# Performance work log

Hardware: AMD Instinct MI355X
Metric: run time of the kernel (lower is better)

The kernel has to match this reference:

```python
import jax, jax.numpy as jnp
import numpy as np

F_CH = 12   # self.f
R = 2       # self.r
LN_EPS = 1e-5


def setup_inputs() -> dict:
    key = jax.random.key(0)
    ks = jax.random.split(key, 12)
    B, C, h, w = 1024, 200, 15, 15
    f, fr = F_CH, F_CH // R
    X = jax.random.normal(ks[0], (B, C, h, w), dtype=jnp.float32)
    # 1x1 conv weights stored as [out, in]; biases [out]
    s_in = 1.0 / np.sqrt(C)
    w11 = jax.random.normal(ks[1], (f, C), dtype=jnp.float32) * s_in
    b11 = jax.random.normal(ks[2], (f,), dtype=jnp.float32) * 0.01
    w21 = jax.random.normal(ks[3], (f, C), dtype=jnp.float32) * s_in
    b21 = jax.random.normal(ks[4], (f,), dtype=jnp.float32) * 0.01
    w31 = jax.random.normal(ks[5], (f, C), dtype=jnp.float32) * s_in
    b31 = jax.random.normal(ks[6], (f,), dtype=jnp.float32) * 0.01
    w41 = jax.random.normal(ks[7], (fr, f), dtype=jnp.float32) * (1.0 / np.sqrt(f))
    b41 = jax.random.normal(ks[8], (fr,), dtype=jnp.float32) * 0.01
    w42 = jax.random.normal(ks[9], (C, fr), dtype=jnp.float32) * (1.0 / np.sqrt(fr))
    b42 = jax.random.normal(ks[10], (C,), dtype=jnp.float32) * 0.01
    ln_g = jnp.ones((C,), dtype=jnp.float32)
    ln_b = jnp.zeros((C,), dtype=jnp.float32)
    return {"X": X, "w11": w11, "b11": b11, "w21": w21, "b21": b21,
            "w31": w31, "b31": b31, "w41": w41, "b41": b41,
            "w42": w42, "b42": b42, "ln_g": ln_g, "ln_b": ln_b}


def reference(X, w11, b11, w21, b21, w31, b31, w41, b41, w42, b42, ln_g, ln_b):
    B, C, h, w = X.shape
    f = F_CH
    HW = h * w
    Xf = X.reshape(B, C, HW)                       # flatten spatial for 1x1 convs
    k = jnp.einsum('bcn,fc->bfn', Xf, w11) + b11[:, None]   # [B,f,HW]
    q = jnp.einsum('bcn,fc->bfn', Xf, w21) + b21[:, None]
    kq = k * q                                               # [B,f,HW]
    v = jnp.einsum('bcn,fc->bfn', Xf, w31) + b31[:, None]    # [B,f,HW]
    # original: permute to [B,h,w,f] then raw reshape to [B,f,1,HW] (scrambles data)
    vp = jnp.transpose(v.reshape(B, f, h, w), (0, 2, 3, 1)).reshape(B, f, HW)
    vm = jnp.mean(vp, axis=-1)                               # adaptive avg pool -> [B,f]
    vs = jax.nn.softmax(vm, axis=1)                          # nn.Softmax default dim=1 on 4D
    # einsum 'bkij,blik->bijl' with i=1: out[b,j,l] = (sum_k kq[b,k,j]) * vs[b,l]
    kqs = jnp.sum(kq, axis=1)                                # [B,HW]
    x41 = kqs[:, :, None] * vs[:, None, :]                   # [B,HW,f]
    x = x41 @ w41.T + b41                                    # conv41: [B,HW,f//r]
    x = x @ w42.T + b42                                      # conv42: [B,HW,C]
    mu = jnp.mean(x, axis=-1, keepdims=True)
    var = jnp.var(x, axis=-1, keepdims=True)
    xn = (x - mu) / jnp.sqrt(var + LN_EPS) * ln_g + ln_b     # LayerNorm(C)
    x42 = jax.nn.sigmoid(jax.nn.relu(xn))                    # [B,HW,C]
    gate = jnp.transpose(x42, (0, 2, 1)).reshape(B, C, h, w)
    return gate * X
```

## Files before the change

kernel.cpp:

```cpp
#include <hip/hip_runtime.h>
#include <math.h>

#define F_CH 12
#define C_DIM 200
#define HW 225
#define PERB (C_DIM*HW)
#define PERB4 (PERB/4)
#define LN_EPS 1e-5f

#define WS_WT   0
#define WS_DP   7200
#define WS_VARD 7400

__global__ __launch_bounds__(256) void k_prep(
    const float* __restrict__ w11, const float* __restrict__ w21,
    const float* __restrict__ w31, const float* __restrict__ b41,
    const float* __restrict__ w42, const float* __restrict__ b42,
    float* __restrict__ wT, float* __restrict__ Dp, float* __restrict__ varD)
{
    const int tid = threadIdx.x;
    for (int i = tid; i < 36*C_DIM; i += 256) {
        int c = i / 36, g = i - 36*c;
        float v;
        if (g < 12)      v = w11[g*C_DIM + c];
        else if (g < 24) v = w21[(g-12)*C_DIM + c];
        else             v = w31[(g-24)*C_DIM + c];
        wT[i] = v;
    }
    __shared__ float red[12];
    __shared__ float DmSh;
    float d = 0.f;
    if (tid < C_DIM) {
        float s = b42[tid];
#pragma unroll
        for (int j = 0; j < 6; ++j) s = fmaf(w42[tid*6+j], b41[j], s);
        d = s;
    }
    float s0 = d;
    for (int o = 32; o > 0; o >>= 1) s0 += __shfl_down(s0, o, 64);
    if ((tid & 63) == 0) red[tid >> 6] = s0;
    __syncthreads();
    if (tid == 0) DmSh = (red[0]+red[1]+red[2]+red[3]) * (1.f/C_DIM);
    __syncthreads();
    float dp = (tid < C_DIM) ? (d - DmSh) : 0.f;
    if (tid < C_DIM) Dp[tid] = dp;
    float s1 = dp*dp;
    for (int o = 32; o > 0; o >>= 1) s1 += __shfl_down(s1, o, 64);
    if ((tid & 63) == 0) red[4 + (tid >> 6)] = s1;
    __syncthreads();
    if (tid == 0) varD[0] = (red[4]+red[5]+red[6]+red[7]) * (1.f/C_DIM);
}

__global__ __launch_bounds__(256) void k_main(
    const float* __restrict__ X,
    const float* __restrict__ wT,
    const float* __restrict__ b11, const float* __restrict__ b21,
    const float* __restrict__ b31,
    const float* __restrict__ w41,
    const float* __restrict__ w42,
    const float* __restrict__ Dp, const float* __restrict__ varDp,
    const float* __restrict__ ln_g, const float* __restrict__ ln_b,
    float* __restrict__ out)
{
    const int b   = blockIdx.x;
    const int tid = threadIdx.x;

    __shared__ float kqsS[HW];
    __shared__ float vmb[F_CH];
    __shared__ float vsS[F_CH];
    __shared__ float t1S[6];
    __shared__ float red[12];
    __shared__ float AmSh, varASh, covSh;
    __shared__ float AgS[C_DIM], DgS[C_DIM], blS[C_DIM];
    __shared__ float PS[HW], RS[HW];

    const float varD = varDp[0];

    float accK[F_CH], accQ[F_CH], accV[F_CH];
#pragma unroll
    for (int f = 0; f < F_CH; ++f) { accK[f] = b11[f]; accQ[f] = b21[f]; accV[f] = b31[f]; }

    const int n = (tid < HW) ? tid : (HW-1);
    const float* xcol = X + (size_t)b*PERB + n;
    for (int c = 0; c < C_DIM; ++c) {
        float x = xcol[c*HW];
        const float* wr = wT + c*36;
#pragma unroll
        for (int f = 0; f < F_CH; ++f) {
            accK[f] = fmaf(x, wr[f],      accK[f]);
            accQ[f] = fmaf(x, wr[12+f],   accQ[f]);
            accV[f] = fmaf(x, wr[24+f],   accV[f]);
        }
    }

    if (tid < F_CH) vmb[tid] = 0.f;
    if (tid < HW) {
        float s = 0.f;
#pragma unroll
        for (int f = 0; f < F_CH; ++f) s = fmaf(accK[f], accQ[f], s);
        kqsS[tid] = s;
    }
    __syncthreads();

    if (tid < HW) {
        int m0 = 12*tid;
        int a0 = m0/225, a1 = (m0+11)/225;
        if (a0 == a1) {
            float s = 0.f;
#pragma unroll
            for (int f = 0; f < F_CH; ++f) s += accV[f];
            atomicAdd(&vmb[a0], s);
        } else {
            int split = 225*a1 - m0;
            float sa = 0.f, sb = 0.f;
#pragma unroll
            for (int f = 0; f < F_CH; ++f) { if (f < split) sa += accV[f]; else sb += accV[f]; }
            atomicAdd(&vmb[a0], sa);
            atomicAdd(&vmb[a1], sb);
        }
    }
    __syncthreads();

    if (tid == 0) {
        float v[F_CH], mx = -1e30f;
#pragma unroll
        for (int a = 0; a < F_CH; ++a) { v[a] = vmb[a]*(1.f/HW); mx = fmaxf(mx, v[a]); }
        float s = 0.f;
#pragma unroll
        for (int a = 0; a < F_CH; ++a) { v[a] = __expf(v[a]-mx); s += v[a]; }
        float inv = 1.f/s;
#pragma unroll
        for (int a = 0; a < F_CH; ++a) vsS[a] = v[a]*inv;
    }
    __syncthreads();

    if (tid < 6) {
        float s = 0.f;
#pragma unroll
        for (int l = 0; l < F_CH; ++l) s = fmaf(w41[tid*F_CH+l], vsS[l], s);
        t1S[tid] = s;
    }
    __syncthreads();

    float A = 0.f, AD = 0.f;
    if (tid < C_DIM) {
        float s = 0.f;
#pragma unroll
        for (int j = 0; j < 6; ++j) s = fmaf(w42[tid*6+j], t1S[j], s);
        A = s;
        AD = A * Dp[tid];
    }
    float r0 = A, r1 = A*A, r2 = AD;
    for (int o = 32; o > 0; o >>= 1) {
        r0 += __shfl_down(r0, o, 64);
        r1 += __shfl_down(r1, o, 64);
        r2 += __shfl_down(r2, o, 64);
    }
    if ((tid & 63) == 0) { int w = tid>>6; red[w*3]=r0; red[w*3+1]=r1; red[w*3+2]=r2; }
    __syncthreads();
    if (tid == 0) {
        float S0 = red[0]+red[3]+red[6]+red[9];
        float S1 = red[1]+red[4]+red[7]+red[10];
        float S2 = red[2]+red[5]+red[8]+red[11];
        float Am = S0*(1.f/C_DIM);
        AmSh   = Am;
        varASh = S1*(1.f/C_DIM) - Am*Am;
        covSh  = S2*(1.f/C_DIM);
    }
    __syncthreads();

    if (tid < C_DIM) {
        float Ap = A - AmSh;
        float g  = ln_g[tid];
        AgS[tid] = Ap*g;
        DgS[tid] = Dp[tid]*g;
        blS[tid] = ln_b[tid];
    }
    if (tid < HW) {
        float kq  = kqsS[tid];
        float var = fmaf(kq*kq, varASh, fmaf(2.f*kq, covSh, varD));
        float rs  = rsqrtf(var + LN_EPS);
        PS[tid] = kq*rs;
        RS[tid] = rs;
    }
    __syncthreads();

    const float4* __restrict__ X4 = (const float4*)(X + (size_t)b*PERB);
    float4* __restrict__ O4 = (float4*)(out + (size_t)b*PERB);
    for (int i = tid; i < PERB4; i += 256) {
        float4 xv = X4[i];
        float xs[4] = {xv.x, xv.y, xv.z, xv.w};
        float rs4[4];
        unsigned base = (unsigned)i*4u;
#pragma unroll
        for (int e = 0; e < 4; ++e) {
            unsigned idx = base + e;
            unsigned c  = idx / HW;
            unsigned nn = idx - c*HW;
            float xn = fmaf(PS[nn], AgS[c], fmaf(RS[nn], DgS[c], blS[c]));
            float gate = (xn > 0.f) ? (1.f/(1.f+__expf(-xn))) : 0.5f;
            rs4[e] = gate * xs[e];
        }
        float4 ov; ov.x=rs4[0]; ov.y=rs4[1]; ov.z=rs4[2]; ov.w=rs4[3];
        O4[i] = ov;
    }
}

extern "C" void kernel_launch(void* const* d_in, const int* in_sizes, int n_in,
                              void* d_out, int out_size, void* d_ws, size_t ws_size,
                              hipStream_t stream) {
    const float* X   = (const float*)d_in[0];
    const float* w11 = (const float*)d_in[1];
    const float* b11 = (const float*)d_in[2];
    const float* w21 = (const float*)d_in[3];
    const float* b21 = (const float*)d_in[4];
    const float* w31 = (const float*)d_in[5];
    const float* b31 = (const float*)d_in[6];
    const float* w41 = (const float*)d_in[7];
    const float* b41 = (const float*)d_in[8];
    const float* w42 = (const float*)d_in[9];
    const float* b42 = (const float*)d_in[10];
    const float* lng = (const float*)d_in[11];
    const float* lnb = (const float*)d_in[12];
    float* out = (float*)d_out;
    float* ws  = (float*)d_ws;

    float* wT = ws + WS_WT;
    float* Dp = ws + WS_DP;
    float* vD = ws + WS_VARD;

    hipLaunchKernelGGL(k_prep, dim3(1), dim3(256), 0, stream,
                       w11, w21, w31, b41, w42, b42, wT, Dp, vD);
    hipLaunchKernelGGL(k_main, dim3(1024), dim3(256), 0, stream,
                       X, wT, b11, b21, b31, w41, w42, Dp, vD, lng, lnb, out);
}
```

Measured before the change: 399.8 us.

## Split fused kernel into conv-stats and channel-split gating kernels

Splits the per-batch fused kernel into two. k_conv computes the projections, with 4-channel unrolling and prefetch of the next X values, and writes per-position and per-channel LayerNorm parameters to workspace. k_gate then launches four blocks per batch, each gating a quarter of the channels with per-thread column loads that avoid the per-element integer division. This aims for more parallelism and better latency hiding in the bandwidth-bound gating pass. The cost is a second read of X from HBM or cache and an extra launch, and it relies on the workspace being large enough, falling back to the old kernel otherwise.

After: 393.2 us. No clear change (-1.7%).

```diff
diff --git a/kernel.cpp b/kernel.cpp
--- a/kernel.cpp
+++ b/kernel.cpp
@@ -10,13 +10,22 @@
 
 #define WS_WT   0
 #define WS_DP   7200
-#define WS_VARD 7400
+#define WS_DG   7400
+#define WS_VARD 7600
+#define WS_PAR  7616
+#define PSTRIDE 656
+#define WS_NEEDED_BYTES ((size_t)(WS_PAR + PSTRIDE*1024) * 4)
+
+#define CSPL 4
+#define CPB  (C_DIM/CSPL)
 
 __global__ __launch_bounds__(256) void k_prep(
     const float* __restrict__ w11, const float* __restrict__ w21,
     const float* __restrict__ w31, const float* __restrict__ b41,
     const float* __restrict__ w42, const float* __restrict__ b42,
-    float* __restrict__ wT, float* __restrict__ Dp, float* __restrict__ varD)
+    const float* __restrict__ ln_g,
+    float* __restrict__ wT, float* __restrict__ Dp, float* __restrict__ Dg,
+    float* __restrict__ varD)
 {
     const int tid = threadIdx.x;
     for (int i = tid; i < 36*C_DIM; i += 256) {
@@ -43,12 +52,194 @@
     if (tid == 0) DmSh = (red[0]+red[1]+red[2]+red[3]) * (1.f/C_DIM);
     __syncthreads();
     float dp = (tid < C_DIM) ? (d - DmSh) : 0.f;
-    if (tid < C_DIM) Dp[tid] = dp;
+    if (tid < C_DIM) { Dp[tid] = dp; Dg[tid] = dp * ln_g[tid]; }
     float s1 = dp*dp;
     for (int o = 32; o > 0; o >>= 1) s1 += __shfl_down(s1, o, 64);
     if ((tid & 63) == 0) red[4 + (tid >> 6)] = s1;
     __syncthreads();
     if (tid == 0) varD[0] = (red[4]+red[5]+red[6]+red[7]) * (1.f/C_DIM);
+}
+
+__global__ __launch_bounds__(256) void k_conv(
+    const float* __restrict__ X,
+    const float* __restrict__ wT,
+    const float* __restrict__ b11, const float* __restrict__ b21,
+    const float* __restrict__ b31,
+    const float* __restrict__ w41,
+    const float* __restrict__ w42,
+    const float* __restrict__ Dp, const float* __restrict__ varDp,
+    const float* __restrict__ ln_g,
+    float* __restrict__ par)
+{
+    const int b   = blockIdx.x;
+    const int tid = threadIdx.x;
+
+    __shared__ float vmb[F_CH];
+    __shared__ float vsS[F_CH];
+    __shared__ float t1S[6];
+    __shared__ float red[12];
+    __shared__ float AmSh, varASh, covSh;
+
+    const float varD = varDp[0];
+
+    float accK[F_CH], accQ[F_CH], accV[F_CH];
+#pragma unroll
+    for (int f = 0; f < F_CH; ++f) { accK[f] = b11[f]; accQ[f] = b21[f]; accV[f] = b31[f]; }
+
+    const int n = (tid < HW) ? tid : (HW-1);
+    const float* xcol = X + (size_t)b*PERB + n;
+
+    float x0 = xcol[0], x1 = xcol[HW], x2 = xcol[2*HW], x3 = xcol[3*HW];
+    for (int c = 0; c < C_DIM; c += 4) {
+        float y0 = 0.f, y1 = 0.f, y2 = 0.f, y3 = 0.f;
+        if (c + 4 < C_DIM) {
+            const float* xn4 = xcol + (size_t)(c+4)*HW;
+            y0 = xn4[0]; y1 = xn4[HW]; y2 = xn4[2*HW]; y3 = xn4[3*HW];
+        }
+        const float* wr = wT + c*36;
+#pragma unroll
+        for (int f = 0; f < F_CH; ++f) {
+            accK[f] = fmaf(x0, wr[f],       accK[f]);
+            accQ[f] = fmaf(x0, wr[12+f],    accQ[f]);
+            accV[f] = fmaf(x0, wr[24+f],    accV[f]);
+            accK[f] = fmaf(x1, wr[36+f],    accK[f]);
+            accQ[f] = fmaf(x1, wr[48+f],    accQ[f]);
+            accV[f] = fmaf(x1, wr[60+f],    accV[f]);
+            accK[f] = fmaf(x2, wr[72+f],    accK[f]);
+            accQ[f] = fmaf(x2, wr[84+f],    accQ[f]);
+            accV[f] = fmaf(x2, wr[96+f],    accV[f]);
+            accK[f] = fmaf(x3, wr[108+f],   accK[f]);
+            accQ[f] = fmaf(x3, wr[120+f],   accQ[f]);
+            accV[f] = fmaf(x3, wr[132+f],   accV[f]);
+        }
+        x0 = y0; x1 = y1; x2 = y2; x3 = y3;
+    }
+
+    float kq = 0.f;
+#pragma unroll
+    for (int f = 0; f < F_CH; ++f) kq = fmaf(accK[f], accQ[f], kq);
+
+    if (tid < F_CH) vmb[tid] = 0.f;
+    __syncthreads();
+
+    if (tid < HW) {
+        int m0 = 12*tid;
+        int a0 = m0/225, a1 = (m0+11)/225;
+        if (a0 == a1) {
+            float s = 0.f;
+#pragma unroll
+            for (int f = 0; f < F_CH; ++f) s += accV[f];
+            atomicAdd(&vmb[a0], s);
+        } else {
+            int split = 225*a1 - m0;
+            float sa = 0.f, sb = 0.f;
+#pragma unroll
+            for (int f = 0; f < F_CH; ++f) { if (f < split) sa += accV[f]; else sb += accV[f]; }
+            atomicAdd(&vmb[a0], sa);
+            atomicAdd(&vmb[a1], sb);
+        }
+    }
+    __syncthreads();
+
+    if (tid == 0) {
+        float v[F_CH], mx = -1e30f;
+#pragma unroll
+        for (int a = 0; a < F_CH; ++a) { v[a] = vmb[a]*(1.f/HW); mx = fmaxf(mx, v[a]); }
+        float s = 0.f;
+#pragma unroll
+        for (int a = 0; a < F_CH; ++a) { v[a] = __expf(v[a]-mx); s += v[a]; }
+        float inv = 1.f/s;
+#pragma unroll
+        for (int a = 0; a < F_CH; ++a) vsS[a] = v[a]*inv;
+    }
+    __syncthreads();
+
+    if (tid < 6) {
+        float s = 0.f;
+#pragma unroll
+        for (int l = 0; l < F_CH; ++l) s = fmaf(w41[tid*F_CH+l], vsS[l], s);
+        t1S[tid] = s;
+    }
+    __syncthreads();
+
+    float A = 0.f, AD = 0.f;
+    if (tid < C_DIM) {
+        float s = 0.f;
+#pragma unroll
+        for (int j = 0; j < 6; ++j) s = fmaf(w42[tid*6+j], t1S[j], s);
+        A = s;
+        AD = A * Dp[tid];
+    }
+    float r0 = A, r1 = A*A, r2 = AD;
+    for (int o = 32; o > 0; o >>= 1) {
+        r0 += __shfl_down(r0, o, 64);
+        r1 += __shfl_down(r1, o, 64);
+        r2 += __shfl_down(r2, o, 64);
+    }
+    if ((tid & 63) == 0) { int w = tid>>6; red[w*3]=r0; red[w*3+1]=r1; red[w*3+2]=r2; }
+    __syncthreads();
+    if (tid == 0) {
+        float S0 = red[0]+red[3]+red[6]+red[9];
+        float S1 = red[1]+red[4]+red[7]+red[10];
+        float S2 = red[2]+red[5]+red[8]+red[11];
+        float Am = S0*(1.f/C_DIM);
+        AmSh   = Am;
+        varASh = S1*(1.f/C_DIM) - Am*Am;
+        covSh  = S2*(1.f/C_DIM);
+    }
+    __syncthreads();
+
+    float* __restrict__ pb = par + (size_t)b*PSTRIDE;
+    if (tid < C_DIM) pb[450+tid] = (A - AmSh) * ln_g[tid];
+    if (tid < HW) {
+        float var = fmaf(kq*kq, varASh, fmaf(2.f*kq, covSh, varD));
+        float rs  = rsqrtf(var + LN_EPS);
+        pb[tid]      = kq*rs;
+        pb[HW+tid]   = rs;
+    }
+}
+
+__global__ __launch_bounds__(256) void k_gate(
+    const float* __restrict__ X,
+    const float* __restrict__ par,
+    const float* __restrict__ Dg, const float* __restrict__ ln_b,
+    float* __restrict__ out)
+{
+    const int blk = blockIdx.x;
+    const int b   = blk >> 2;
+    const int seg = blk & 3;
+    const int c0  = seg * CPB;
+    const int tid = threadIdx.x;
+
+    __shared__ float AgL[CPB], DgL[CPB], blL[CPB];
+
+    const float* __restrict__ pb = par + (size_t)b*PSTRIDE;
+    if (tid < CPB) {
+        int c = c0 + tid;
+        AgL[tid] = pb[450+c];
+        DgL[tid] = Dg[c];
+        blL[tid] = ln_b[c];
+    }
+    float pn = 0.f, rn = 0.f;
+    if (tid < HW) { pn = pb[tid]; rn = pb[HW+tid]; }
+    __syncthreads();
+
+    if (tid < HW) {
+        const float* __restrict__ xb = X   + (size_t)b*PERB + (size_t)c0*HW + tid;
+        float*       __restrict__ ob = out + (size_t)b*PERB + (size_t)c0*HW + tid;
+        for (int j0 = 0; j0 < CPB; j0 += 5) {
+            float xv[5];
+#pragma unroll
+            for (int u = 0; u < 5; ++u) xv[u] = xb[(size_t)(j0+u)*HW];
+#pragma unroll
+            for (int u = 0; u < 5; ++u) {
+                int j = j0 + u;
+                float xn   = fmaf(pn, AgL[j], fmaf(rn, DgL[j], blL[j]));
+                float gate = (xn > 0.f) ? (1.f/(1.f+__expf(-xn))) : 0.5f;
+                ob[(size_t)j*HW] = gate * xv[u];
+            }
+        }
+    }
 }
 
 __global__ __launch_bounds__(256) void k_main(
@@ -227,10 +418,20 @@
 
     float* wT = ws + WS_WT;
     float* Dp = ws + WS_DP;
+    float* Dg = ws + WS_DG;
     float* vD = ws + WS_VARD;
+    float* par = ws + WS_PAR;
 
     hipLaunchKernelGGL(k_prep, dim3(1), dim3(256), 0, stream,
-                       w11, w21, w31, b41, w42, b42, wT, Dp, vD);
-    hipLaunchKernelGGL(k_main, dim3(1024), dim3(256), 0, stream,
-                       X, wT, b11, b21, b31, w41, w42, Dp, vD, lng, lnb, out);
+                       w11, w21, w31, b41, w42, b42, lng, wT, Dp, Dg, vD);
+
+    if (ws_size >= WS_NEEDED_BYTES) {
+        hipLaunchKernelGGL(k_conv, dim3(1024), dim3(256), 0, stream,
+                           X, wT, b11, b21, b31, w41, w42, Dp, vD, lng, par);
+        hipLaunchKernelGGL(k_gate, dim3(1024*CSPL), dim3(256), 0, stream,
+                           X, par, Dg, lnb, out);
+    } else {
+        hipLaunchKernelGGL(k_main, dim3(1024), dim3(256), 0, stream,
+                           X, wT, b11, b21, b31, w41, w42, Dp, vD, lng, lnb, out);
+    }
 }
```

## Prefetch X in conv loop and keep per-pixel LN stats in registers for output

Applied to the files above, without the earlier changes.

The 1x1-conv channel loop now software-pipelines X loads two 4-channel groups ahead. The kq value and the per-pixel LN scale stay in registers, which removes the PS/RS/kqs shared arrays. The output pass switches from a float4 flat loop to a per-pixel loop over channels with non-temporal stores, which drops the integer div/mod and adds launch_bounds occupancy hints. The trade-off is that only 225 of 256 threads are active in the output phase, and scalar stores replace vector stores.

New measurement: 385.0 us. 3.7% less time.

```diff
diff --git a/kernel.cpp b/kernel.cpp
--- a/kernel.cpp
+++ b/kernel.cpp
@@ -5,7 +5,6 @@
 #define C_DIM 200
 #define HW 225
 #define PERB (C_DIM*HW)
-#define PERB4 (PERB/4)
 #define LN_EPS 1e-5f
 
 #define WS_WT   0
@@ -51,7 +50,7 @@
     if (tid == 0) varD[0] = (red[4]+red[5]+red[6]+red[7]) * (1.f/C_DIM);
 }
 
-__global__ __launch_bounds__(256) void k_main(
+__global__ __launch_bounds__(256, 4) void k_fused(
     const float* __restrict__ X,
     const float* __restrict__ wT,
     const float* __restrict__ b11, const float* __restrict__ b21,
@@ -65,14 +64,12 @@
     const int b   = blockIdx.x;
     const int tid = threadIdx.x;
 
-    __shared__ float kqsS[HW];
     __shared__ float vmb[F_CH];
     __shared__ float vsS[F_CH];
     __shared__ float t1S[6];
     __shared__ float red[12];
     __shared__ float AmSh, varASh, covSh;
     __shared__ float AgS[C_DIM], DgS[C_DIM], blS[C_DIM];
-    __shared__ float PS[HW], RS[HW];
 
     const float varD = varDp[0];
 
@@ -82,24 +79,46 @@
 
     const int n = (tid < HW) ? tid : (HW-1);
     const float* xcol = X + (size_t)b*PERB + n;
-    for (int c = 0; c < C_DIM; ++c) {
-        float x = xcol[c*HW];
-        const float* wr = wT + c*36;
-#pragma unroll
-        for (int f = 0; f < F_CH; ++f) {
-            accK[f] = fmaf(x, wr[f],      accK[f]);
-            accQ[f] = fmaf(x, wr[12+f],   accQ[f]);
-            accV[f] = fmaf(x, wr[24+f],   accV[f]);
-        }
-    }
+
+#define CONV_STEP(CBASE, XR)                                              \
+    {                                                                     \
+        const float* wr_ = wT + (CBASE)*36;                               \
+        _Pragma("unroll")                                                 \
+        for (int u = 0; u < 4; ++u) {                                     \
+            float xv_ = XR[u];                                            \
+            const float* wu_ = wr_ + u*36;                                \
+            _Pragma("unroll")                                             \
+            for (int f = 0; f < F_CH; ++f) {                              \
+                accK[f] = fmaf(xv_, wu_[f],    accK[f]);                  \
+                accQ[f] = fmaf(xv_, wu_[12+f], accQ[f]);                  \
+                accV[f] = fmaf(xv_, wu_[24+f], accV[f]);                  \
+            }                                                             \
+        }                                                                 \
+    }
+
+    float xA[4], xB[4];
+#pragma unroll
+    for (int u = 0; u < 4; ++u) xA[u] = xcol[(size_t)u*HW];
+#pragma unroll
+    for (int u = 0; u < 4; ++u) xB[u] = xcol[(size_t)(4+u)*HW];
+    for (int c = 0; c < C_DIM - 8; c += 4) {
+        float xC[4];
+        const float* xn4 = xcol + (size_t)(c+8)*HW;
+#pragma unroll
+        for (int u = 0; u < 4; ++u) xC[u] = xn4[(size_t)u*HW];
+        CONV_STEP(c, xA);
+#pragma unroll
+        for (int u = 0; u < 4; ++u) { xA[u] = xB[u]; xB[u] = xC[u]; }
+    }
+    CONV_STEP(C_DIM-8, xA);
+    CONV_STEP(C_DIM-4, xB);
+#undef CONV_STEP
+
+    float kq = 0.f;
+#pragma unroll
+    for (int f = 0; f < F_CH; ++f) kq = fmaf(accK[f], accQ[f], kq);
 
     if (tid < F_CH) vmb[tid] = 0.f;
-    if (tid < HW) {
-        float s = 0.f;
-#pragma unroll
-        for (int f = 0; f < F_CH; ++f) s = fmaf(accK[f], accQ[f], s);
-        kqsS[tid] = s;
-    }
     __syncthreads();
 
     if (tid < HW) {
@@ -170,39 +189,48 @@
     __syncthreads();
 
     if (tid < C_DIM) {
-        float Ap = A - AmSh;
         float g  = ln_g[tid];
-        AgS[tid] = Ap*g;
+        AgS[tid] = (A - AmSh)*g;
         DgS[tid] = Dp[tid]*g;
         blS[tid] = ln_b[tid];
     }
+    float Pn = 0.f, Rn = 0.f;
     if (tid < HW) {
-        float kq  = kqsS[tid];
         float var = fmaf(kq*kq, varASh, fmaf(2.f*kq, covSh, varD));
         float rs  = rsqrtf(var + LN_EPS);
-        PS[tid] = kq*rs;
-        RS[tid] = rs;
-    }
-    __syncthreads();
-
-    const float4* __restrict__ X4 = (const float4*)(X + (size_t)b*PERB);
-    float4* __restrict__ O4 = (float4*)(out + (size_t)b*PERB);
-    for (int i = tid; i < PERB4; i += 256) {
-        float4 xv = X4[i];
-        float xs[4] = {xv.x, xv.y, xv.z, xv.w};
-        float rs4[4];
-        unsigned base = (unsigned)i*4u;
-#pragma unroll
-        for (int e = 0; e < 4; ++e) {
-            unsigned idx = base + e;
-            unsigned c  = idx / HW;
-            unsigned nn = idx - c*HW;
-            float xn = fmaf(PS[nn], AgS[c], fmaf(RS[nn], DgS[c], blS[c]));
+        Pn = kq*rs;
+        Rn = rs;
+    }
+    __syncthreads();
+
+    if (tid < HW) {
+        const float* __restrict__ xb = X   + (size_t)b*PERB + tid;
+        float*       __restrict__ ob = out + (size_t)b*PERB + tid;
+        float v0[4];
+#pragma unroll
+        for (int u = 0; u < 4; ++u) v0[u] = xb[(size_t)u*HW];
+        for (int c = 0; c < C_DIM - 4; c += 4) {
+            float nv[4];
+            const float* xn4 = xb + (size_t)(c+4)*HW;
+#pragma unroll
+            for (int u = 0; u < 4; ++u) nv[u] = xn4[(size_t)u*HW];
+#pragma unroll
+            for (int u = 0; u < 4; ++u) {
+                int cc = c + u;
+                float xn   = fmaf(Pn, AgS[cc], fmaf(Rn, DgS[cc], blS[cc]));
+                float gate = (xn > 0.f) ? (1.f/(1.f+__expf(-xn))) : 0.5f;
+                __builtin_nontemporal_store(gate * v0[u], &ob[(size_t)cc*HW]);
+            }
+#pragma unroll
+            for (int u = 0; u < 4; ++u) v0[u] = nv[u];
+        }
+#pragma unroll
+        for (int u = 0; u < 4; ++u) {
+            int cc = C_DIM - 4 + u;
+            float xn   = fmaf(Pn, AgS[cc], fmaf(Rn, DgS[cc], blS[cc]));
             float gate = (xn > 0.f) ? (1.f/(1.f+__expf(-xn))) : 0.5f;
-            rs4[e] = gate * xs[e];
+            __builtin_nontemporal_store(gate * v0[u], &ob[(size_t)cc*HW]);
         }
-        float4 ov; ov.x=rs4[0]; ov.y=rs4[1]; ov.z=rs4[2]; ov.w=rs4[3];
-        O4[i] = ov;
     }
 }
 
@@ -231,6 +259,6 @@
 
     hipLaunchKernelGGL(k_prep, dim3(1), dim3(256), 0, stream,
                        w11, w21, w31, b41, w42, b42, wT, Dp, vD);
-    hipLaunchKernelGGL(k_main, dim3(1024), dim3(256), 0, stream,
+    hipLaunchKernelGGL(k_fused, dim3(1024), dim3(256), 0, stream,
                        X, wT, b11, b21, b31, w41, w42, Dp, vD, lng, lnb, out);
 }
```
